# Kernel optimization log

Measured on AMD Instinct MI355X. Metric: run time of the kernel, lower is better.

Reference implementation:

```python
import jax, jax.numpy as jnp
import numpy as np

HEAD_SIZE = 256
ROTARY_DIM = 64
ROPE_THETA = 10000.0


def apply_gptj_rope(x, positions):
    """GPT-J (interleaved, non-neox) rotary embedding.
    x: [B, S, H, D], positions: [B, S] int. Rotates first ROTARY_DIM dims."""
    half = ROTARY_DIM // 2
    inv_freq = 1.0 / (ROPE_THETA ** (jnp.arange(0, ROTARY_DIM, 2, dtype=jnp.float32) / ROTARY_DIM))
    ang = positions.astype(jnp.float32)[..., None] * inv_freq      # [B, S, half]
    cos = jnp.cos(ang)[:, :, None, :]                               # [B, S, 1, half]
    sin = jnp.sin(ang)[:, :, None, :]
    xr, xp = x[..., :ROTARY_DIM], x[..., ROTARY_DIM:]
    x1, x2 = xr[..., 0::2], xr[..., 1::2]                           # interleaved pairs
    o1 = x1 * cos - x2 * sin
    o2 = x2 * cos + x1 * sin
    rot = jnp.stack([o1, o2], axis=-1).reshape(*xr.shape)           # re-interleave
    return jnp.concatenate([rot, xp], axis=-1)


def setup_inputs() -> dict:
    key = jax.random.key(0)
    k1, k2, k3 = jax.random.split(key, 3)
    B, S, H = 2, 2048, 4096
    position_ids = jnp.broadcast_to(jnp.arange(S, dtype=jnp.int32), (B, S))
    hidden_states = jax.random.normal(k1, (B, S, H), dtype=jnp.float32)
    Wqkv = jax.random.normal(k2, (H, 3 * H), dtype=jnp.float32) * (H ** -0.5)
    Wo = jax.random.normal(k3, (H, H), dtype=jnp.float32) * (H ** -0.5)
    return {"position_ids": position_ids, "hidden_states": hidden_states, "Wqkv": Wqkv, "Wo": Wo}


def reference(position_ids, hidden_states, Wqkv, Wo):
    B, S, H = hidden_states.shape
    nh = H // HEAD_SIZE
    qkv = hidden_states @ Wqkv                                      # [B, S, 3H]
    q, k, v = jnp.split(qkv, 3, axis=-1)
    q = apply_gptj_rope(q.reshape(B, S, nh, HEAD_SIZE), position_ids)
    k = apply_gptj_rope(k.reshape(B, S, nh, HEAD_SIZE), position_ids)
    v = v.reshape(B, S, nh, HEAD_SIZE)
    scale = HEAD_SIZE ** -0.5
    scores = jnp.einsum('bqhd,bkhd->bhqk', q, k) * scale            # [B, nh, S, S]
    causal = jnp.tril(jnp.ones((S, S), dtype=bool))
    scores = jnp.where(causal, scores, jnp.finfo(scores.dtype).min)
    attn = jax.nn.softmax(scores, axis=-1)
    ctx = jnp.einsum('bhqk,bkhd->bqhd', attn, v).reshape(B, S, H)
    return ctx @ Wo
```

## Files before the change

### kernel.cpp

```cpp
#include <hip/hip_runtime.h>
#include <hip/hip_bf16.h>

typedef __bf16 bf16x8 __attribute__((ext_vector_type(8)));
typedef float f32x4 __attribute__((ext_vector_type(4)));

#define MFMA_BF16(a,b,c) __builtin_amdgcn_mfma_f32_16x16x32_bf16(a,b,c,0,0,0)

#define GLOAD16(g, l) __builtin_amdgcn_global_load_lds( \
    (const __attribute__((address_space(1))) unsigned int*)(g), \
    (__attribute__((address_space(3))) unsigned int*)(l), 16, 0, 0)

__device__ __forceinline__ unsigned short f2bf(float f) {
  unsigned u = __builtin_bit_cast(unsigned, f);
  return (unsigned short)((u + 0x7FFFu + ((u >> 16) & 1u)) >> 16);
}

__global__ __launch_bounds__(256)
void prep_merged(const float* __restrict__ hidden, unsigned short* __restrict__ hiddenB,
                 const float* __restrict__ Wqkv, unsigned short* __restrict__ WqkvT,
                 const float* __restrict__ Wo, unsigned short* __restrict__ WoT) {
  __shared__ float tl[64][65];
  const int id = blockIdx.x;
  const bool hasWo = (WoT != nullptr);
  if (id < 12288) {
    const int n0 = (id % 192) * 64, k0 = (id / 192) * 64;
    const int K = 4096, N = 12288;
    const int tr = threadIdx.x >> 4;
    const int tc4 = (threadIdx.x & 15) * 4;
    for (int i = 0; i < 4; ++i) {
      int r = tr + i*16;
      float4 v = *(const float4*)(Wqkv + (size_t)(k0 + r)*N + n0 + tc4);
      tl[r][tc4+0] = v.x; tl[r][tc4+1] = v.y;
      tl[r][tc4+2] = v.z; tl[r][tc4+3] = v.w;
    }
    __syncthreads();
    for (int i = 0; i < 4; ++i) {
      int nr = tr + i*16;
      short4 h;
      h.x = (short)f2bf(tl[tc4+0][nr]);
      h.y = (short)f2bf(tl[tc4+1][nr]);
      h.z = (short)f2bf(tl[tc4+2][nr]);
      h.w = (short)f2bf(tl[tc4+3][nr]);
      *(short4*)(WqkvT + (size_t)(n0 + nr)*K + k0 + tc4) = h;
    }
  } else if (hasWo && id < 16384) {
    const int id2 = id - 12288;
    const int n0 = (id2 & 63) * 64, k0 = (id2 >> 6) * 64;
    const int K = 4096, N = 4096;
    const int tr = threadIdx.x >> 4;
    const int tc4 = (threadIdx.x & 15) * 4;
    for (int i = 0; i < 4; ++i) {
      int r = tr + i*16;
      float4 v = *(const float4*)(Wo + (size_t)(k0 + r)*N + n0 + tc4);
      tl[r][tc4+0] = v.x; tl[r][tc4+1] = v.y;
      tl[r][tc4+2] = v.z; tl[r][tc4+3] = v.w;
    }
    __syncthreads();
    for (int i = 0; i < 4; ++i) {
      int nr = tr + i*16;
      short4 h;
      h.x = (short)f2bf(tl[tc4+0][nr]);
      h.y = (short)f2bf(tl[tc4+1][nr]);
      h.z = (short)f2bf(tl[tc4+2][nr]);
      h.w = (short)f2bf(tl[tc4+3][nr]);
      *(short4*)(WoT + (size_t)(n0 + nr)*K + k0 + tc4) = h;
    }
  } else {
    const int cbase = hasWo ? 16384 : 12288;
    const int n8 = 4096*4096/8;
    int i = (id - cbase) * 256 + threadIdx.x;
    const int stride = 2048 * 256;
    for (; i < n8; i += stride) {
      float4 a = ((const float4*)hidden)[i*2];
      float4 b = ((const float4*)hidden)[i*2 + 1];
      short4 h0, h1;
      h0.x = (short)f2bf(a.x); h0.y = (short)f2bf(a.y);
      h0.z = (short)f2bf(a.z); h0.w = (short)f2bf(a.w);
      h1.x = (short)f2bf(b.x); h1.y = (short)f2bf(b.y);
      h1.z = (short)f2bf(b.z); h1.w = (short)f2bf(b.w);
      ((short4*)hiddenB)[i*2] = h0;
      ((short4*)hiddenB)[i*2 + 1] = h1;
    }
  }
}

__global__ __launch_bounds__(256)
void transpose_convert(const float* __restrict__ W, unsigned short* __restrict__ Wt,
                       int K, int N) {
  __shared__ float tl[64][65];
  const int k0 = blockIdx.y * 64, n0 = blockIdx.x * 64;
  const int tr = threadIdx.x >> 4;
  const int tc4 = (threadIdx.x & 15) * 4;
  for (int i = 0; i < 4; ++i) {
    int r = tr + i*16;
    float4 v = *(const float4*)(W + (size_t)(k0 + r)*N + n0 + tc4);
    tl[r][tc4+0] = v.x; tl[r][tc4+1] = v.y;
    tl[r][tc4+2] = v.z; tl[r][tc4+3] = v.w;
  }
  __syncthreads();
  for (int i = 0; i < 4; ++i) {
    int nr = tr + i*16;
    short4 h;
    h.x = (short)f2bf(tl[tc4+0][nr]);
    h.y = (short)f2bf(tl[tc4+1][nr]);
    h.z = (short)f2bf(tl[tc4+2][nr]);
    h.w = (short)f2bf(tl[tc4+3][nr]);
    *(short4*)(Wt + (size_t)(n0 + nr)*K + k0 + tc4) = h;
  }
}

__global__ __launch_bounds__(256)
void transpose_v(const unsigned short* __restrict__ qkv,
                 unsigned short* __restrict__ Vt) {
  __shared__ unsigned short tl[64][68];
  const int bh = blockIdx.z;
  const int s0 = blockIdx.x * 64;
  const int d0 = blockIdx.y * 64;
  const int b = bh >> 4, h = bh & 15;
  const int tr = threadIdx.x >> 4;
  const int tc = (threadIdx.x & 15) * 4;
  const unsigned short* src = qkv + ((size_t)(b*2048 + s0))*12288 + 8192 + h*256 + d0;
  for (int i = 0; i < 4; ++i) {
    int s = tr + i*16;
    *(short4*)&tl[s][tc] = *(const short4*)(src + (size_t)s*12288 + tc);
  }
  __syncthreads();
  unsigned short* dst = Vt + ((size_t)bh*256 + d0)*2048 + s0;
  for (int i = 0; i < 4; ++i) {
    int d = tr + i*16;
    short4 h4;
    h4.x = (short)tl[tc+0][d];
    h4.y = (short)tl[tc+1][d];
    h4.z = (short)tl[tc+2][d];
    h4.w = (short)tl[tc+3][d];
    *(short4*)(dst + (size_t)d*2048 + tc) = h4;
  }
}

template<bool ROPE, bool OUT_BF16, bool VFUSE>
__global__ __launch_bounds__(512, 2)
void gemm256p(const unsigned short* __restrict__ A,
              const unsigned short* __restrict__ Bt,
              const int* __restrict__ pos,
              void* __restrict__ Cp, int N, int K, int nrow,
              unsigned short* __restrict__ Vt)
{
  __shared__ __align__(16) unsigned short L[2][4][8192];
  const int tid = threadIdx.x, lane = tid & 63, w = tid >> 6;
  const int wr = w >> 2, wc = w & 3;
  const int nwg = gridDim.x;
  int wg = blockIdx.x;
  if ((nwg & 7) == 0) wg = (wg & 7) * (nwg >> 3) + (wg >> 3);
  const int by = wg % nrow, bx = wg / nrow;
  const int row0 = by * 256, col0 = bx * 256;

  const int crow = lane & 15, g = lane >> 4;
  const int xo = (crow & 7) << 4;
  const int rB0 = (wc & 1) * 64;
  const unsigned bo = (unsigned)((tid >> 3) * K + (((tid & 7) ^ ((tid >> 3) & 7)) * 8));
  const int nt = K >> 6;

#define STG_A(T,BUF,H,RLO) do { if ((T) < nt)                                   \
    GLOAD16(A + (unsigned)((row0 + (H)*128 + (RLO))*K) + bo + (unsigned)(T)*64u,\
            &L[BUF][H][(RLO)*64 + tid*8]); } while (0)
#define STG_B(T,BUF,H,RLO) do { if ((T) < nt)                                   \
    GLOAD16(Bt + (unsigned)((col0 + (H)*128 + (RLO))*K) + bo + (unsigned)(T)*64u,\
            &L[BUF][2+(H)][(RLO)*64 + tid*8]); } while (0)

#define RD_ALO(BUF) _Pragma("unroll") for (int m = 0; m < 4; ++m)               \
    _Pragma("unroll") for (int kk = 0; kk < 2; ++kk)                            \
      pAlo[m][kk] = *(const bf16x8*)((const char*)&L[BUF][wr][0] +              \
                     (m*16 + crow)*128 + ((((kk*4+g)<<4)) ^ xo));
#define RD_AHI(BUF) _Pragma("unroll") for (int m = 0; m < 4; ++m)               \
    _Pragma("unroll") for (int kk = 0; kk < 2; ++kk)                            \
      pAhi[m][kk] = *(const bf16x8*)((const char*)&L[BUF][wr][0] +              \
                     (64 + m*16 + crow)*128 + ((((kk*4+g)<<4)) ^ xo));
#define RD_B0(BUF) _Pragma("unroll") for (int n = 0; n < 2; ++n)                \
    _Pragma("unroll") for (int kk = 0; kk < 2; ++kk)                            \
      pB0[n][kk] = *(const bf16x8*)((const char*)&L[BUF][2+(wc>>1)][0] +        \
                    (rB0 + n*16 + crow)*128 + ((((kk*4+g)<<4)) ^ xo));
#define RD_B1(BUF) _Pragma("unroll") for (int n = 0; n < 2; ++n)                \
    _Pragma("unroll") for (int kk = 0; kk < 2; ++kk)                            \
      pB1[n][kk] = *(const bf16x8*)((const char*)&L[BUF][2+(wc>>1)][0] +        \
                    (rB0 + 32 + n*16 + crow)*128 + ((((kk*4+g)<<4)) ^ xo));
#define Q00 _Pragma("unroll") for (int kk = 0; kk < 2; ++kk)                    \
    _Pragma("unroll") for (int m = 0; m < 4; ++m)                               \
    _Pragma("unroll") for (int n = 0; n < 2; ++n)                               \
      acc[m][n] = MFMA_BF16(pAlo[m][kk], pB0[n][kk], acc[m][n]);
#define Q01 _Pragma("unroll") for (int kk = 0; kk < 2; ++kk)                    \
    _Pragma("unroll") for (int m = 0; m < 4; ++m)                               \
    _Pragma("unroll") for (int n = 0; n < 2; ++n)                               \
      acc[m][2+n] = MFMA_BF16(pAlo[m][kk], pB1[n][kk], acc[m][2+n]);
#define Q10 _Pragma("unroll") for (int kk = 0; kk < 2; ++kk)                    \
    _Pragma("unroll") for (int m = 0; m < 4; ++m)                               \
    _Pragma("unroll") for (int n = 0; n < 2; ++n)                               \
      acc[4+m][n] = MFMA_BF16(pAhi[m][kk], pB0[n][kk], acc[4+m][n]);
#define Q11 _Pragma("unroll") for (int kk = 0; kk < 2; ++kk)                    \
    _Pragma("unroll") for (int m = 0; m < 4; ++m)                               \
    _Pragma("unroll") for (int n = 0; n < 2; ++n)                               \
      acc[4+m][2+n] = MFMA_BF16(pAhi[m][kk], pB1[n][kk], acc[4+m][2+n]);
#define BAR __builtin_amdgcn_s_barrier()
#define LGKM0 asm volatile("s_waitcnt lgkmcnt(0)" ::: "memory")
#define PRIO1 __builtin_amdgcn_s_setprio(1)
#define PRIO0 __builtin_amdgcn_s_setprio(0)

  f32x4 acc[8][4] = {};
  STG_A(0,0,0,0);  STG_A(0,0,0,64); STG_A(0,0,1,0);  STG_A(0,0,1,64);
  STG_B(0,0,0,0);  STG_B(0,0,0,64); STG_B(0,0,1,0);  STG_B(0,0,1,64);
  STG_A(1,1,0,0);  STG_A(1,1,1,0);
  STG_B(1,1,0,0);  STG_B(1,1,0,64); STG_B(1,1,1,0);  STG_B(1,1,1,64);
  asm volatile("s_waitcnt vmcnt(6)" ::: "memory");
  BAR;

  const int nI = nt >> 1;
  for (int i = 0; i < nI; ++i) {
    const int t = 2*i;
    const bool last = (i == nI - 1);
    bf16x8 pAlo[4][2], pAhi[4][2], pB0[2][2], pB1[2][2];

    RD_ALO(0); RD_B0(0);
    STG_A(t+1, 1, 0, 64); STG_A(t+1, 1, 1, 64);
    PRIO1; Q00; PRIO0; LGKM0; BAR;
    RD_B1(0);
    STG_A(t+2, 0, 0, 0); STG_A(t+2, 0, 1, 0);
    PRIO1; Q01; PRIO0; LGKM0; BAR;
    RD_AHI(0);
    STG_B(t+2, 0, 0, 0); STG_B(t+2, 0, 0, 64);
    STG_B(t+2, 0, 1, 0); STG_B(t+2, 0, 1, 64);
    PRIO1; Q10; Q11; PRIO0; LGKM0;
    if (!last) asm volatile("s_waitcnt vmcnt(6)" ::: "memory");
    else       asm volatile("s_waitcnt vmcnt(0)" ::: "memory");
    BAR;

    RD_ALO(1); RD_B0(1);
    STG_A(t+2, 0, 0, 64); STG_A(t+2, 0, 1, 64);
    PRIO1; Q00; PRIO0; LGKM0; BAR;
    RD_B1(1);
    STG_A(t+3, 1, 0, 0); STG_A(t+3, 1, 1, 0);
    PRIO1; Q01; PRIO0; LGKM0; BAR;
    RD_AHI(1);
    STG_B(t+3, 1, 0, 0); STG_B(t+3, 1, 0, 64);
    STG_B(t+3, 1, 1, 0); STG_B(t+3, 1, 1, 64);
    PRIO1; Q10; Q11; PRIO0; LGKM0;
    if (!last) asm volatile("s_waitcnt vmcnt(6)" ::: "memory");
    else       asm volatile("s_waitcnt vmcnt(0)" ::: "memory");
    BAR;
  }
#undef STG_A
#undef STG_B
#undef RD_ALO
#undef RD_AHI
#undef RD_B0
#undef RD_B1
#undef Q00
#undef Q01
#undef Q10
#undef Q11
#undef BAR
#undef LGKM0
#undef PRIO1
#undef PRIO0

  if (VFUSE && ROPE && col0 >= 8192) {
#pragma unroll
    for (int m = 0; m < 8; ++m) {
      const int rbase = row0 + wr*128 + m*16 + (g << 2);
      const int b = rbase >> 11, s0 = rbase & 2047;
#pragma unroll
      for (int n = 0; n < 4; ++n) {
        const int d = col0 - 8192 + wc*64 + n*16 + crow;
        short4 hv;
        hv.x = (short)f2bf(acc[m][n][0]);
        hv.y = (short)f2bf(acc[m][n][1]);
        hv.z = (short)f2bf(acc[m][n][2]);
        hv.w = (short)f2bf(acc[m][n][3]);
        *(short4*)(Vt + ((size_t)(b*4096 + d))*2048 + s0) = hv;
      }
    }
    return;
  }

#pragma unroll
  for (int m = 0; m < 8; ++m) {
    const int rbase = row0 + wr*128 + m*16 + (g << 2);
#pragma unroll
    for (int n = 0; n < 4; ++n) {
      const int c = col0 + wc*64 + n*16 + crow;
      bool rot = false;
      float invf = 0.f;
      if (ROPE) {
        rot = (c < 8192) && ((c & 255) < 64);
        if (rot) {
          int i2 = (c & 63) >> 1;
          invf = exp2f(-(float)i2 * 0.4152410118609203f);
        }
      }
#pragma unroll
      for (int r = 0; r < 4; ++r) {
        int rowg = rbase + r;
        float v = acc[m][n][r];
        if (ROPE && rot) {
          float ang = (float)pos[rowg] * invf;
          float s_ = __sinf(ang), c_ = __cosf(ang);
          float pv = __shfl_xor(v, 1, 64);
          v = (c & 1) ? fmaf(v, c_, pv * s_) : fmaf(v, c_, -pv * s_);
        }
        if (OUT_BF16)
          ((unsigned short*)Cp)[(size_t)rowg*N + c] = f2bf(v);
        else
          ((float*)Cp)[(size_t)rowg*N + c] = v;
      }
    }
  }
}

template<bool A_BF16, bool ROPE, bool OUT_BF16>
__global__ __launch_bounds__(256)
void gemm128(const void* __restrict__ Ap, const float* __restrict__ Bp,
             const int* __restrict__ pos, void* __restrict__ Cp,
             int N, int K)
{
  __shared__ __align__(16) short Al[128*40];
  __shared__ __align__(16) short Bl[128*40];
  const int tid = threadIdx.x;
  const int lane = tid & 63, wid = tid >> 6;
  const int wr = wid >> 1, wc = wid & 1;
  const int row0 = blockIdx.y * 128, col0 = blockIdx.x * 128;
  f32x4 acc[4][4] = {};
  const int bcol = tid & 127;
  const int kb0 = (tid >> 7) * 4;

  for (int kt = 0; kt < K; kt += 32) {
    if (A_BF16) {
      const unsigned short* Ab = (const unsigned short*)Ap;
      for (int i = 0; i < 2; ++i) {
        int idx = tid + i*256;
        int ar = idx >> 2, ac = (idx & 3) * 8;
        *(int4*)(&Al[ar*40 + ac]) = *(const int4*)(Ab + (size_t)(row0+ar)*K + kt + ac);
      }
    } else {
      const float* Af = (const float*)Ap;
      for (int i = 0; i < 4; ++i) {
        int idx = tid + i*256;
        int ar = idx >> 3, ac = (idx & 7) * 4;
        float4 v = *(const float4*)(Af + (size_t)(row0+ar)*K + kt + ac);
        short4 h;
        h.x = (short)f2bf(v.x); h.y = (short)f2bf(v.y);
        h.z = (short)f2bf(v.z); h.w = (short)f2bf(v.w);
        *(short4*)(&Al[ar*40 + ac]) = h;
      }
    }
    for (int r = 0; r < 4; ++r) {
      int kb = kb0 + r*8;
      const float* bp = Bp + (size_t)(kt+kb)*N + col0 + bcol;
      float x0 = bp[0];
      float x1 = bp[(size_t)N];
      float x2 = bp[2*(size_t)N];
      float x3 = bp[3*(size_t)N];
      short4 h;
      h.x = (short)f2bf(x0); h.y = (short)f2bf(x1);
      h.z = (short)f2bf(x2); h.w = (short)f2bf(x3);
      *(short4*)(&Bl[bcol*40 + kb]) = h;
    }
    __syncthreads();
    const int k8 = (lane >> 4) * 8;
    bf16x8 af[4], bfr[4];
    for (int m = 0; m < 4; ++m)
      af[m] = *(const bf16x8*)(&Al[(wr*64 + m*16 + (lane&15))*40 + k8]);
    for (int n = 0; n < 4; ++n)
      bfr[n] = *(const bf16x8*)(&Bl[(wc*64 + n*16 + (lane&15))*40 + k8]);
    for (int m = 0; m < 4; ++m)
      for (int n = 0; n < 4; ++n)
        acc[m][n] = MFMA_BF16(af[m], bfr[n], acc[m][n]);
    __syncthreads();
  }

  for (int m = 0; m < 4; ++m) {
    const int rbase = row0 + wr*64 + m*16 + ((lane>>4)<<2);
    for (int n = 0; n < 4; ++n) {
      const int c = col0 + wc*64 + n*16 + (lane & 15);
      bool rot = false;
      float invf = 0.f;
      if (ROPE) {
        rot = (c < 8192) && ((c & 255) < 64);
        if (rot) {
          int i2 = (c & 63) >> 1;
          invf = exp2f(-(float)i2 * 0.4152410118609203f);
        }
      }
      for (int r = 0; r < 4; ++r) {
        int rowg = rbase + r;
        float v = acc[m][n][r];
        if (ROPE && rot) {
          float ang = (float)pos[rowg] * invf;
          float s_ = __sinf(ang), c_ = __cosf(ang);
          float pv = __shfl_xor(v, 1, 64);
          v = (c & 1) ? fmaf(v, c_, pv * s_) : fmaf(v, c_, -pv * s_);
        }
        if (OUT_BF16)
          ((unsigned short*)Cp)[(size_t)rowg*N + c] = f2bf(v);
        else
          ((float*)Cp)[(size_t)rowg*N + c] = v;
      }
    }
  }
}

__global__ __launch_bounds__(512, 2)
void attn_kernel3(const unsigned short* __restrict__ qkv,
                  const unsigned short* __restrict__ Vt,
                  unsigned short* __restrict__ ctx)
{
  const int QN = 12288;
  __shared__ __align__(16) unsigned char Kl[2][32768];
  __shared__ __align__(16) unsigned char Vl[2][32768];
  __shared__ __align__(16) unsigned char Pl[128*144];
  const int tid = threadIdx.x, lane = tid & 63, w = tid >> 6;
  const int qp = blockIdx.x, bh = blockIdx.y;
  const int b = bh >> 4, h = bh & 15;
  const size_t rowbase = (size_t)b * 2048;
  const int colr = lane & 15, g = lane >> 4;

  const int kr0 = tid >> 5;
  const int kcolb = ((tid*16) & 511) ^ ((kr0 & 7) << 4);
  const unsigned koff = (unsigned)(kr0*QN) + (kcolb >> 1);
  const int vd0 = tid >> 3;
  const int vcolb = ((tid*16) & 127) ^ ((vd0 & 7) << 4);
  const unsigned voff = (unsigned)(vd0*2048) + (vcolb >> 1);

  const unsigned short* kbase = qkv + rowbase*QN + 4096 + h*256;
  const unsigned short* vbase = Vt + (size_t)bh*256*2048;

#define STAGEKV(KT, B) do {                                                    \
    const unsigned short* kb_ = kbase + (unsigned)(KT)*64u*(unsigned)QN;       \
    const unsigned short* vb_ = vbase + (unsigned)(KT)*64u;                    \
    _Pragma("unroll")                                                          \
    for (int i = 0; i < 4; ++i)                                                \
      GLOAD16(kb_ + koff + i*16*QN, &Kl[B][tid*16 + i*8192]);                  \
    _Pragma("unroll")                                                          \
    for (int i = 0; i < 4; ++i)                                                \
      GLOAD16(vb_ + voff + i*64*2048, &Vl[B][tid*16 + i*8192]);                \
  } while (0)

  for (int phase = 0; phase < 2; ++phase) {
    const int qt = phase ? qp : (15 - qp);
    const int nkt = 2*qt + 2;

    bf16x8 qf[8];
    {
      const unsigned short* qp_ = qkv + (rowbase + qt*128 + w*16 + colr)*QN + h*256 + g*8;
#pragma unroll
      for (int f = 0; f < 8; ++f)
        qf[f] = *(const bf16x8*)(qp_ + 32*f);
    }
    f32x4 acc[16] = {};
    float m_r[4], l_r[4];
#pragma unroll
    for (int r = 0; r < 4; ++r) { m_r[r] = -1e30f; l_r[r] = 0.f; }

    STAGEKV(0, 0);
    STAGEKV(1, 1);
    int cur = 0;

    for (int kt = 0; kt < nkt; ++kt) {
      if (kt < nkt - 1) asm volatile("s_waitcnt vmcnt(8)" ::: "memory");
      else              asm volatile("s_waitcnt vmcnt(0)" ::: "memory");
      __builtin_amdgcn_s_barrier();

      const unsigned char* Kb = Kl[cur];
      f32x4 sc[4];
      __builtin_amdgcn_s_setprio(1);
#pragma unroll
      for (int nf = 0; nf < 4; ++nf) {
        f32x4 s = {};
        int krow = nf*16 + colr;
        int xo2 = (krow & 7) << 4;
        const unsigned char* kp = Kb + krow*512;
#pragma unroll
        for (int st = 0; st < 8; ++st) {
          bf16x8 kf = *(const bf16x8*)(kp + ((64*st + 16*g) ^ xo2));
          s = MFMA_BF16(qf[st], kf, s);
        }
        sc[nf] = s;
      }
      __builtin_amdgcn_s_setprio(0);

      const int qrow0 = qt*128 + w*16 + g*4;
      float pm[4] = {-3e38f,-3e38f,-3e38f,-3e38f};
      float pvv[4][4];
#pragma unroll
      for (int nf = 0; nf < 4; ++nf) {
        int kcol = kt*64 + nf*16 + colr;
#pragma unroll
        for (int r = 0; r < 4; ++r) {
          float v = sc[nf][r] * 0.0625f;
          if (kcol > qrow0 + r) v = -1e30f;
          pvv[nf][r] = v;
          pm[r] = fmaxf(pm[r], v);
        }
      }
#pragma unroll
      for (int mk = 1; mk < 16; mk <<= 1)
#pragma unroll
        for (int r = 0; r < 4; ++r)
          pm[r] = fmaxf(pm[r], __shfl_xor(pm[r], mk, 64));
      float alpha[4];
#pragma unroll
      for (int r = 0; r < 4; ++r) {
        float mn = fmaxf(m_r[r], pm[r]);
        alpha[r] = __expf(m_r[r] - mn);
        m_r[r] = mn;
      }
      float ps[4] = {0.f,0.f,0.f,0.f};
      unsigned short pb[4][4];
#pragma unroll
      for (int nf = 0; nf < 4; ++nf)
#pragma unroll
        for (int r = 0; r < 4; ++r) {
          float p = __expf(pvv[nf][r] - m_r[r]);
          ps[r] += p;
          pb[nf][r] = f2bf(p);
        }
#pragma unroll
      for (int mk = 1; mk < 16; mk <<= 1)
#pragma unroll
        for (int r = 0; r < 4; ++r)
          ps[r] += __shfl_xor(ps[r], mk, 64);
#pragma unroll
      for (int r = 0; r < 4; ++r)
        l_r[r] = l_r[r]*alpha[r] + ps[r];
#pragma unroll
      for (int nf2 = 0; nf2 < 16; ++nf2)
#pragma unroll
        for (int r = 0; r < 4; ++r)
          acc[nf2][r] *= alpha[r];

#pragma unroll
      for (int nf = 0; nf < 4; ++nf)
#pragma unroll
        for (int r = 0; r < 4; ++r)
          *(unsigned short*)(Pl + (w*16 + g*4 + r)*144 + (nf*16 + colr)*2) = pb[nf][r];

      const unsigned char* Vb = Vl[cur];
      __builtin_amdgcn_s_setprio(1);
#pragma unroll
      for (int st2 = 0; st2 < 2; ++st2) {
        bf16x8 pf = *(const bf16x8*)(Pl + (w*16 + colr)*144 + (32*st2 + g*8)*2);
#pragma unroll
        for (int nf2 = 0; nf2 < 16; ++nf2) {
          int d = nf2*16 + colr;
          bf16x8 vf = *(const bf16x8*)(Vb + ((d*128 + 64*st2 + 16*g) ^ ((d&7)<<4)));
          acc[nf2] = MFMA_BF16(pf, vf, acc[nf2]);
        }
      }
      __builtin_amdgcn_s_setprio(0);

      __builtin_amdgcn_sched_barrier(0);
      asm volatile("s_waitcnt lgkmcnt(0)" ::: "memory");
      __builtin_amdgcn_sched_barrier(0);
      __builtin_amdgcn_s_barrier();
      if (kt + 2 < nkt) STAGEKV(kt + 2, cur);
      cur ^= 1;
    }

    float linv[4];
#pragma unroll
    for (int r = 0; r < 4; ++r) linv[r] = 1.0f / l_r[r];
#pragma unroll
    for (int nf2 = 0; nf2 < 16; ++nf2)
#pragma unroll
      for (int r = 0; r < 4; ++r) {
        int qrow = qt*128 + w*16 + g*4 + r;
        float o = acc[nf2][r] * linv[r];
        ctx[(rowbase + qrow)*4096 + h*256 + nf2*16 + colr] = f2bf(o);
      }
  }
#undef STAGEKV
}

__global__ __launch_bounds__(256, 2)
void attn_kernel2(const unsigned short* __restrict__ qkv,
                  unsigned short* __restrict__ ctx)
{
  const int S = 2048, D = 256, QN = 12288;
  __shared__ __align__(16) unsigned char Kl[64*512];
  __shared__ __align__(16) unsigned char Vl[256*128];
  __shared__ __align__(16) unsigned char Pl[64*144];
  const int tid = threadIdx.x, lane = tid & 63, w = tid >> 6;
  const int qp = blockIdx.x, bh = blockIdx.y;
  const int b = bh >> 4, h = bh & 15;
  const size_t rowbase = (size_t)b * S;
  const int colr = lane & 15, g = lane >> 4;

  const int kr0 = tid >> 5, c8 = (tid & 31) * 8;
  const unsigned kwb = (unsigned)((kr0*512 + c8*2) ^ ((kr0 & 7) << 4));
  const int dd = (tid >> 2) * 4, kbb = (tid & 3) * 4;

  const unsigned short* kbase0 = qkv + rowbase*QN + 4096 + h*D;
  const unsigned short* vbase0 = qkv + rowbase*QN + 8192 + h*D;

  bf16x8 kreg[8];
  short4 vreg[16];

#define LOADKV(KT) do {                                                        \
    const unsigned short* kb_ = kbase0 + (size_t)(KT)*64*QN;                   \
    _Pragma("unroll")                                                          \
    for (int i = 0; i < 8; ++i)                                                \
      kreg[i] = *(const bf16x8*)(kb_ + (size_t)(kr0 + i*8)*QN + c8);           \
    const unsigned short* vb_ = vbase0 + (size_t)(KT)*64*QN;                   \
    _Pragma("unroll")                                                          \
    for (int r4 = 0; r4 < 4; ++r4) {                                           \
      int kb2 = kbb + 16*r4;                                                   \
      _Pragma("unroll")                                                        \
      for (int j = 0; j < 4; ++j)                                              \
        vreg[r4*4+j] = *(const short4*)(vb_ + (size_t)(kb2+j)*QN + dd);        \
    }                                                                          \
  } while (0)

#define WRITEKV() do {                                                         \
    _Pragma("unroll")                                                          \
    for (int i = 0; i < 8; ++i)                                                \
      *(bf16x8*)(Kl + kwb + i*4096) = kreg[i];                                 \
    _Pragma("unroll")                                                          \
    for (int r4 = 0; r4 < 4; ++r4) {                                           \
      int kb2 = kbb + 16*r4;                                                   \
      short4 v0 = vreg[r4*4+0], v1 = vreg[r4*4+1];                             \
      short4 v2 = vreg[r4*4+2], v3 = vreg[r4*4+3];                             \
      short4 t;                                                                \
      t.x=v0.x; t.y=v1.x; t.z=v2.x; t.w=v3.x;                                  \
      *(short4*)(Vl + (((dd+0)*128 + kb2*2) ^ (((dd+0)&7)<<4))) = t;           \
      t.x=v0.y; t.y=v1.y; t.z=v2.y; t.w=v3.y;                                  \
      *(short4*)(Vl + (((dd+1)*128 + kb2*2) ^ (((dd+1)&7)<<4))) = t;           \
      t.x=v0.z; t.y=v1.z; t.z=v2.z; t.w=v3.z;                                  \
      *(short4*)(Vl + (((dd+2)*128 + kb2*2) ^ (((dd+2)&7)<<4))) = t;           \
      t.x=v0.w; t.y=v1.w; t.z=v2.w; t.w=v3.w;                                  \
      *(short4*)(Vl + (((dd+3)*128 + kb2*2) ^ (((dd+3)&7)<<4))) = t;           \
    }                                                                          \
  } while (0)

  for (int phase = 0; phase < 2; ++phase) {
    const int qt = phase ? qp : (31 - qp);

    bf16x8 qf[8];
    {
      const unsigned short* qp_ = qkv + (rowbase + qt*64 + w*16 + colr)*QN + h*D + g*8;
#pragma unroll
      for (int f = 0; f < 8; ++f)
        qf[f] = *(const bf16x8*)(qp_ + 32*f);
    }
    f32x4 acc[16] = {};
    float m_r[4], l_r[4];
#pragma unroll
    for (int r = 0; r < 4; ++r) { m_r[r] = -1e30f; l_r[r] = 0.f; }

    LOADKV(0);
    WRITEKV();
    __syncthreads();

    for (int kt = 0; kt <= qt; ++kt) {
      if (kt < qt) LOADKV(kt + 1);
      __builtin_amdgcn_sched_barrier(0);

      f32x4 sc[4];
#pragma unroll
      for (int nf = 0; nf < 4; ++nf) {
        f32x4 s = {};
        int krow = nf*16 + colr;
        int xo2 = (krow & 7) << 4;
        const unsigned char* kp = Kl + krow*512;
#pragma unroll
        for (int st = 0; st < 8; ++st) {
          bf16x8 kf = *(const bf16x8*)(kp + ((64*st + 16*g) ^ xo2));
          s = MFMA_BF16(qf[st], kf, s);
        }
        sc[nf] = s;
      }

      const int qrow0 = qt*64 + w*16 + g*4;
      float pm[4] = {-3e38f,-3e38f,-3e38f,-3e38f};
      float pvv[4][4];
#pragma unroll
      for (int nf = 0; nf < 4; ++nf) {
        int kcol = kt*64 + nf*16 + colr;
#pragma unroll
        for (int r = 0; r < 4; ++r) {
          float v = sc[nf][r] * 0.0625f;
          if (kcol > qrow0 + r) v = -1e30f;
          pvv[nf][r] = v;
          pm[r] = fmaxf(pm[r], v);
        }
      }
#pragma unroll
      for (int mk = 1; mk < 16; mk <<= 1)
#pragma unroll
        for (int r = 0; r < 4; ++r)
          pm[r] = fmaxf(pm[r], __shfl_xor(pm[r], mk, 64));
      float alpha[4];
#pragma unroll
      for (int r = 0; r < 4; ++r) {
        float mn = fmaxf(m_r[r], pm[r]);
        alpha[r] = __expf(m_r[r] - mn);
        m_r[r] = mn;
      }
      float ps[4] = {0.f,0.f,0.f,0.f};
      unsigned short pb[4][4];
#pragma unroll
      for (int nf = 0; nf < 4; ++nf)
#pragma unroll
        for (int r = 0; r < 4; ++r) {
          float p = __expf(pvv[nf][r] - m_r[r]);
          ps[r] += p;
          pb[nf][r] = f2bf(p);
        }
#pragma unroll
      for (int mk = 1; mk < 16; mk <<= 1)
#pragma unroll
        for (int r = 0; r < 4; ++r)
          ps[r] += __shfl_xor(ps[r], mk, 64);
#pragma unroll
      for (int r = 0; r < 4; ++r)
        l_r[r] = l_r[r]*alpha[r] + ps[r];
#pragma unroll
      for (int nf2 = 0; nf2 < 16; ++nf2)
#pragma unroll
        for (int r = 0; r < 4; ++r)
          acc[nf2][r] *= alpha[r];

#pragma unroll
      for (int nf = 0; nf < 4; ++nf)
#pragma unroll
        for (int r = 0; r < 4; ++r)
          *(unsigned short*)(Pl + (w*16 + g*4 + r)*144 + (nf*16 + colr)*2) = pb[nf][r];

#pragma unroll
      for (int st2 = 0; st2 < 2; ++st2) {
        bf16x8 pf = *(const bf16x8*)(Pl + (w*16 + colr)*144 + (32*st2 + g*8)*2);
#pragma unroll
        for (int nf2 = 0; nf2 < 16; ++nf2) {
          int d = nf2*16 + colr;
          bf16x8 vf = *(const bf16x8*)(Vl + ((d*128 + 64*st2 + 16*g) ^ ((d&7)<<4)));
          acc[nf2] = MFMA_BF16(pf, vf, acc[nf2]);
        }
      }
      __syncthreads();
      if (kt < qt) {
        WRITEKV();
        __syncthreads();
      }
    }

    float linv[4];
#pragma unroll
    for (int r = 0; r < 4; ++r) linv[r] = 1.0f / l_r[r];
#pragma unroll
    for (int nf2 = 0; nf2 < 16; ++nf2)
#pragma unroll
      for (int r = 0; r < 4; ++r) {
        int qrow = qt*64 + w*16 + g*4 + r;
        float o = acc[nf2][r] * linv[r];
        ctx[(rowbase + qrow)*4096 + h*D + nf2*16 + colr] = f2bf(o);
      }
    if (phase == 0) __syncthreads();
  }
#undef LOADKV
#undef WRITEKV
}

extern "C" void kernel_launch(void* const* d_in, const int* in_sizes, int n_in,
                              void* d_out, int out_size, void* d_ws, size_t ws_size,
                              hipStream_t stream) {
  const int*   pos    = (const int*)d_in[0];
  const float* hidden = (const float*)d_in[1];
  const float* Wqkv   = (const float*)d_in[2];
  const float* Wo     = (const float*)d_in[3];

  const size_t QKV_B  = (size_t)4096 * 12288 * 2;
  const size_t CTX_B  = (size_t)4096 * 4096 * 2;
  const size_t VT_B   = (size_t)32 * 256 * 2048 * 2;
  const size_t WO_B   = (size_t)4096 * 4096 * 2;
  const size_t FAST_NEED = QKV_B + QKV_B + CTX_B;

  if (ws_size >= FAST_NEED) {
    unsigned short* qkv     = (unsigned short*)d_ws;
    unsigned short* WqkvT   = (unsigned short*)((char*)d_ws + QKV_B);
    unsigned short* ctx     = (unsigned short*)((char*)d_ws + QKV_B + CTX_B);
    unsigned short* hiddenB = (unsigned short*)((char*)d_ws + 2*QKV_B);

    const bool vfuse  = ws_size >= FAST_NEED + VT_B;
    const bool wofuse = ws_size >= FAST_NEED + VT_B + WO_B;
    unsigned short* Vt  = vfuse ? (unsigned short*)((char*)d_ws + FAST_NEED)
                                : hiddenB;
    unsigned short* WoT = wofuse ? (unsigned short*)((char*)d_ws + FAST_NEED + VT_B)
                                 : WqkvT;

    prep_merged<<<wofuse ? 18432 : 14336, 256, 0, stream>>>(
        hidden, hiddenB, Wqkv, WqkvT,
        wofuse ? Wo : nullptr, wofuse ? WoT : nullptr);
    if (vfuse)
      gemm256p<true, true, true><<<768, 512, 0, stream>>>(
          hiddenB, WqkvT, pos, qkv, 12288, 4096, 16, Vt);
    else
      gemm256p<true, true, false><<<768, 512, 0, stream>>>(
          hiddenB, WqkvT, pos, qkv, 12288, 4096, 16, nullptr);
    if (!wofuse)
      transpose_convert<<<dim3(64, 64), 256, 0, stream>>>(Wo, WoT, 4096, 4096);
    if (!vfuse)
      transpose_v<<<dim3(32, 4, 32), 256, 0, stream>>>(qkv, Vt);
    attn_kernel3<<<dim3(8, 32), 512, 0, stream>>>(qkv, Vt, ctx);
    gemm256p<false, false, false><<<256, 512, 0, stream>>>(
        ctx, WoT, nullptr, d_out, 4096, 4096, 16, nullptr);
  } else {
    if (ws_size < QKV_B + CTX_B) return;
    unsigned short* qkv = (unsigned short*)d_ws;
    unsigned short* ctx = qkv + (size_t)4096 * 12288;
    gemm128<false, true, true><<<dim3(96, 32), 256, 0, stream>>>(
        hidden, Wqkv, pos, qkv, 12288, 4096);
    attn_kernel2<<<dim3(16, 32), 256, 0, stream>>>(qkv, ctx);
    gemm128<true, false, false><<<dim3(32, 32), 256, 0, stream>>>(
        ctx, Wo, nullptr, d_out, 4096, 4096);
  }
}
```

Measured before the change: 712.7 us.

## Make QKV GEMM persistent with three column tiles per workgroup

The QKV projection GEMM now launches 256 workgroups instead of 768, and each one loops over three 256-wide column tiles spaced by a column stride. The global-to-LDS prologue loads for the next tile are issued right after the current tile's epilogue, so the next tile's prefetch overlaps the epilogue stores. The goal is to avoid the tail wave caused by 768 blocks on 256 CUs and to reuse the same A row block across tiles. In exchange the kernel is more complex, and load balance or L2 locality may change since each block now covers columns across Q, K and V.

```diff
diff --git a/kernel.cpp b/kernel.cpp
--- a/kernel.cpp
+++ b/kernel.cpp
@@ -142,7 +142,7 @@
 void gemm256p(const unsigned short* __restrict__ A,
               const unsigned short* __restrict__ Bt,
               const int* __restrict__ pos,
-              void* __restrict__ Cp, int N, int K, int nrow,
+              void* __restrict__ Cp, int N, int K, int nrow, int nrep,
               unsigned short* __restrict__ Vt)
 {
   __shared__ __align__(16) unsigned short L[2][4][8192];
@@ -151,8 +151,9 @@
   const int nwg = gridDim.x;
   int wg = blockIdx.x;
   if ((nwg & 7) == 0) wg = (wg & 7) * (nwg >> 3) + (wg >> 3);
-  const int by = wg % nrow, bx = wg / nrow;
-  const int row0 = by * 256, col0 = bx * 256;
+  const int by = wg % nrow, bx0 = wg / nrow;
+  const int row0 = by * 256;
+  const int colstep = (nwg / nrow) * 256;
 
   const int crow = lane & 15, g = lane >> 4;
   const int xo = (crow & 7) << 4;
@@ -163,9 +164,18 @@
 #define STG_A(T,BUF,H,RLO) do { if ((T) < nt)                                   \
     GLOAD16(A + (unsigned)((row0 + (H)*128 + (RLO))*K) + bo + (unsigned)(T)*64u,\
             &L[BUF][H][(RLO)*64 + tid*8]); } while (0)
-#define STG_B(T,BUF,H,RLO) do { if ((T) < nt)                                   \
-    GLOAD16(Bt + (unsigned)((col0 + (H)*128 + (RLO))*K) + bo + (unsigned)(T)*64u,\
+#define STG_B(C0,T,BUF,H,RLO) do { if ((T) < nt)                                \
+    GLOAD16(Bt + (unsigned)(((C0) + (H)*128 + (RLO))*K) + bo + (unsigned)(T)*64u,\
             &L[BUF][2+(H)][(RLO)*64 + tid*8]); } while (0)
+
+#define PROLOGUE(C0) do {                                                      \
+    STG_A(0,0,0,0);  STG_A(0,0,0,64); STG_A(0,0,1,0);  STG_A(0,0,1,64);        \
+    STG_B(C0,0,0,0,0);  STG_B(C0,0,0,0,64);                                    \
+    STG_B(C0,0,0,1,0);  STG_B(C0,0,0,1,64);                                    \
+    STG_A(1,1,0,0);  STG_A(1,1,1,0);                                           \
+    STG_B(C0,1,1,0,0);  STG_B(C0,1,1,0,64);                                    \
+    STG_B(C0,1,1,1,0);  STG_B(C0,1,1,1,64);                                    \
+  } while (0)
 
 #define RD_ALO(BUF) _Pragma("unroll") for (int m = 0; m < 4; ++m)               \
     _Pragma("unroll") for (int kk = 0; kk < 2; ++kk)                            \
@@ -204,50 +214,106 @@
 #define PRIO1 __builtin_amdgcn_s_setprio(1)
 #define PRIO0 __builtin_amdgcn_s_setprio(0)
 
-  f32x4 acc[8][4] = {};
-  STG_A(0,0,0,0);  STG_A(0,0,0,64); STG_A(0,0,1,0);  STG_A(0,0,1,64);
-  STG_B(0,0,0,0);  STG_B(0,0,0,64); STG_B(0,0,1,0);  STG_B(0,0,1,64);
-  STG_A(1,1,0,0);  STG_A(1,1,1,0);
-  STG_B(1,1,0,0);  STG_B(1,1,0,64); STG_B(1,1,1,0);  STG_B(1,1,1,64);
-  asm volatile("s_waitcnt vmcnt(6)" ::: "memory");
-  BAR;
-
-  const int nI = nt >> 1;
-  for (int i = 0; i < nI; ++i) {
-    const int t = 2*i;
-    const bool last = (i == nI - 1);
-    bf16x8 pAlo[4][2], pAhi[4][2], pB0[2][2], pB1[2][2];
-
-    RD_ALO(0); RD_B0(0);
-    STG_A(t+1, 1, 0, 64); STG_A(t+1, 1, 1, 64);
-    PRIO1; Q00; PRIO0; LGKM0; BAR;
-    RD_B1(0);
-    STG_A(t+2, 0, 0, 0); STG_A(t+2, 0, 1, 0);
-    PRIO1; Q01; PRIO0; LGKM0; BAR;
-    RD_AHI(0);
-    STG_B(t+2, 0, 0, 0); STG_B(t+2, 0, 0, 64);
-    STG_B(t+2, 0, 1, 0); STG_B(t+2, 0, 1, 64);
-    PRIO1; Q10; Q11; PRIO0; LGKM0;
-    if (!last) asm volatile("s_waitcnt vmcnt(6)" ::: "memory");
-    else       asm volatile("s_waitcnt vmcnt(0)" ::: "memory");
+  PROLOGUE(bx0 * 256);
+
+  for (int rep = 0; rep < nrep; ++rep) {
+    const int col0 = bx0 * 256 + rep * colstep;
+
+    asm volatile("s_waitcnt vmcnt(6)" ::: "memory");
     BAR;
 
-    RD_ALO(1); RD_B0(1);
-    STG_A(t+2, 0, 0, 64); STG_A(t+2, 0, 1, 64);
-    PRIO1; Q00; PRIO0; LGKM0; BAR;
-    RD_B1(1);
-    STG_A(t+3, 1, 0, 0); STG_A(t+3, 1, 1, 0);
-    PRIO1; Q01; PRIO0; LGKM0; BAR;
-    RD_AHI(1);
-    STG_B(t+3, 1, 0, 0); STG_B(t+3, 1, 0, 64);
-    STG_B(t+3, 1, 1, 0); STG_B(t+3, 1, 1, 64);
-    PRIO1; Q10; Q11; PRIO0; LGKM0;
-    if (!last) asm volatile("s_waitcnt vmcnt(6)" ::: "memory");
-    else       asm volatile("s_waitcnt vmcnt(0)" ::: "memory");
-    BAR;
+    f32x4 acc[8][4] = {};
+    const int nI = nt >> 1;
+    for (int i = 0; i < nI; ++i) {
+      const int t = 2*i;
+      const bool last = (i == nI - 1);
+      bf16x8 pAlo[4][2], pAhi[4][2], pB0[2][2], pB1[2][2];
+
+      RD_ALO(0); RD_B0(0);
+      STG_A(t+1, 1, 0, 64); STG_A(t+1, 1, 1, 64);
+      PRIO1; Q00; PRIO0; LGKM0; BAR;
+      RD_B1(0);
+      STG_A(t+2, 0, 0, 0); STG_A(t+2, 0, 1, 0);
+      PRIO1; Q01; PRIO0; LGKM0; BAR;
+      RD_AHI(0);
+      STG_B(col0, t+2, 0, 0, 0); STG_B(col0, t+2, 0, 0, 64);
+      STG_B(col0, t+2, 0, 1, 0); STG_B(col0, t+2, 0, 1, 64);
+      PRIO1; Q10; Q11; PRIO0; LGKM0;
+      if (!last) asm volatile("s_waitcnt vmcnt(6)" ::: "memory");
+      else       asm volatile("s_waitcnt vmcnt(0)" ::: "memory");
+      BAR;
+
+      RD_ALO(1); RD_B0(1);
+      STG_A(t+2, 0, 0, 64); STG_A(t+2, 0, 1, 64);
+      PRIO1; Q00; PRIO0; LGKM0; BAR;
+      RD_B1(1);
+      STG_A(t+3, 1, 0, 0); STG_A(t+3, 1, 1, 0);
+      PRIO1; Q01; PRIO0; LGKM0; BAR;
+      RD_AHI(1);
+      STG_B(col0, t+3, 1, 0, 0); STG_B(col0, t+3, 1, 0, 64);
+      STG_B(col0, t+3, 1, 1, 0); STG_B(col0, t+3, 1, 1, 64);
+      PRIO1; Q10; Q11; PRIO0; LGKM0;
+      if (!last) asm volatile("s_waitcnt vmcnt(6)" ::: "memory");
+      else       asm volatile("s_waitcnt vmcnt(0)" ::: "memory");
+      BAR;
+    }
+
+    if (VFUSE && ROPE && col0 >= 8192) {
+#pragma unroll
+      for (int m = 0; m < 8; ++m) {
+        const int rbase = row0 + wr*128 + m*16 + (g << 2);
+        const int b = rbase >> 11, s0 = rbase & 2047;
+#pragma unroll
+        for (int n = 0; n < 4; ++n) {
+          const int d = col0 - 8192 + wc*64 + n*16 + crow;
+          short4 hv;
+          hv.x = (short)f2bf(acc[m][n][0]);
+          hv.y = (short)f2bf(acc[m][n][1]);
+          hv.z = (short)f2bf(acc[m][n][2]);
+          hv.w = (short)f2bf(acc[m][n][3]);
+          *(short4*)(Vt + ((size_t)(b*4096 + d))*2048 + s0) = hv;
+        }
+      }
+    } else {
+#pragma unroll
+      for (int m = 0; m < 8; ++m) {
+        const int rbase = row0 + wr*128 + m*16 + (g << 2);
+#pragma unroll
+        for (int n = 0; n < 4; ++n) {
+          const int c = col0 + wc*64 + n*16 + crow;
+          bool rot = false;
+          float invf = 0.f;
+          if (ROPE) {
+            rot = (c < 8192) && ((c & 255) < 64);
+            if (rot) {
+              int i2 = (c & 63) >> 1;
+              invf = exp2f(-(float)i2 * 0.4152410118609203f);
+            }
+          }
+#pragma unroll
+          for (int r = 0; r < 4; ++r) {
+            int rowg = rbase + r;
+            float v = acc[m][n][r];
+            if (ROPE && rot) {
+              float ang = (float)pos[rowg] * invf;
+              float s_ = __sinf(ang), c_ = __cosf(ang);
+              float pv = __shfl_xor(v, 1, 64);
+              v = (c & 1) ? fmaf(v, c_, pv * s_) : fmaf(v, c_, -pv * s_);
+            }
+            if (OUT_BF16)
+              ((unsigned short*)Cp)[(size_t)rowg*N + c] = f2bf(v);
+            else
+              ((float*)Cp)[(size_t)rowg*N + c] = v;
+          }
+        }
+      }
+    }
+
+    if (rep + 1 < nrep) PROLOGUE(col0 + colstep);
   }
 #undef STG_A
 #undef STG_B
+#undef PROLOGUE
 #undef RD_ALO
 #undef RD_AHI
 #undef RD_B0
@@ -260,58 +326,6 @@
 #undef LGKM0
 #undef PRIO1
 #undef PRIO0
-
-  if (VFUSE && ROPE && col0 >= 8192) {
-#pragma unroll
-    for (int m = 0; m < 8; ++m) {
-      const int rbase = row0 + wr*128 + m*16 + (g << 2);
-      const int b = rbase >> 11, s0 = rbase & 2047;
-#pragma unroll
-      for (int n = 0; n < 4; ++n) {
-        const int d = col0 - 8192 + wc*64 + n*16 + crow;
-        short4 hv;
-        hv.x = (short)f2bf(acc[m][n][0]);
-        hv.y = (short)f2bf(acc[m][n][1]);
-        hv.z = (short)f2bf(acc[m][n][2]);
-        hv.w = (short)f2bf(acc[m][n][3]);
-        *(short4*)(Vt + ((size_t)(b*4096 + d))*2048 + s0) = hv;
-      }
-    }
-    return;
-  }
-
-#pragma unroll
-  for (int m = 0; m < 8; ++m) {
-    const int rbase = row0 + wr*128 + m*16 + (g << 2);
-#pragma unroll
-    for (int n = 0; n < 4; ++n) {
-      const int c = col0 + wc*64 + n*16 + crow;
-      bool rot = false;
-      float invf = 0.f;
-      if (ROPE) {
-        rot = (c < 8192) && ((c & 255) < 64);
-        if (rot) {
-          int i2 = (c & 63) >> 1;
-          invf = exp2f(-(float)i2 * 0.4152410118609203f);
-        }
-      }
-#pragma unroll
-      for (int r = 0; r < 4; ++r) {
-        int rowg = rbase + r;
-        float v = acc[m][n][r];
-        if (ROPE && rot) {
-          float ang = (float)pos[rowg] * invf;
-          float s_ = __sinf(ang), c_ = __cosf(ang);
-          float pv = __shfl_xor(v, 1, 64);
-          v = (c & 1) ? fmaf(v, c_, pv * s_) : fmaf(v, c_, -pv * s_);
-        }
-        if (OUT_BF16)
-          ((unsigned short*)Cp)[(size_t)rowg*N + c] = f2bf(v);
-        else
-          ((float*)Cp)[(size_t)rowg*N + c] = v;
-      }
-    }
-  }
 }
 
 template<bool A_BF16, bool ROPE, bool OUT_BF16>
@@ -797,18 +811,18 @@
         hidden, hiddenB, Wqkv, WqkvT,
         wofuse ? Wo : nullptr, wofuse ? WoT : nullptr);
     if (vfuse)
-      gemm256p<true, true, true><<<768, 512, 0, stream>>>(
-          hiddenB, WqkvT, pos, qkv, 12288, 4096, 16, Vt);
+      gemm256p<true, true, true><<<256, 512, 0, stream>>>(
+          hiddenB, WqkvT, pos, qkv, 12288, 4096, 16, 3, Vt);
     else
-      gemm256p<true, true, false><<<768, 512, 0, stream>>>(
-          hiddenB, WqkvT, pos, qkv, 12288, 4096, 16, nullptr);
+      gemm256p<true, true, false><<<256, 512, 0, stream>>>(
+          hiddenB, WqkvT, pos, qkv, 12288, 4096, 16, 3, nullptr);
     if (!wofuse)
       transpose_convert<<<dim3(64, 64), 256, 0, stream>>>(Wo, WoT, 4096, 4096);
     if (!vfuse)
       transpose_v<<<dim3(32, 4, 32), 256, 0, stream>>>(qkv, Vt);
     attn_kernel3<<<dim3(8, 32), 512, 0, stream>>>(qkv, Vt, ctx);
     gemm256p<false, false, false><<<256, 512, 0, stream>>>(
-        ctx, WoT, nullptr, d_out, 4096, 4096, 16, nullptr);
+        ctx, WoT, nullptr, d_out, 4096, 4096, 16, 1, nullptr);
   } else {
     if (ws_size < QKV_B + CTX_B) return;
     unsigned short* qkv = (unsigned short*)d_ws;
```

After: 785.6 us. +10.2%, slower.
